# Kernel tuning notes

Hardware: AMD Instinct MI355X
Metric: run time of the kernel (lower is better)

## Reference

```python
import jax, jax.numpy as jnp
import numpy as np

DIM = 128
NUM_HEADS = 4
WS = (2, 7, 7)  # window size (D, H, W)
N = WS[0] * WS[1] * WS[2]  # 98 tokens per window
NW = 64    # number of windows per sample (mask.shape[0])
BATCH = 64
B_ = BATCH * NW


def _relative_position_index(ws):
    # replicates the numpy index construction in build()
    coords = np.stack(np.meshgrid(np.arange(ws[0]), np.arange(ws[1]), np.arange(ws[2]), indexing='ij'))
    flat = coords.reshape(3, -1)  # (3, N)
    rel = flat[:, :, None] - flat[:, None, :]  # (3, N, N)
    rel = rel.transpose(1, 2, 0).astype(np.int64)
    rel[:, :, 0] += ws[0] - 1
    rel[:, :, 1] += ws[1] - 1
    rel[:, :, 2] += ws[2] - 1
    rel[:, :, 0] *= (2 * ws[1] - 1) * (2 * ws[2] - 1)
    rel[:, :, 1] *= 2 * ws[2] - 1
    return rel.sum(-1)  # (N, N)


def setup_inputs() -> dict:
    key = jax.random.key(0)
    ks = jax.random.split(key, 8)
    C = DIM
    num_bias = (2 * WS[0] - 1) * (2 * WS[1] - 1) * (2 * WS[2] - 1)  # 507
    x = jax.random.normal(ks[0], (B_, N, C), dtype=jnp.float32)
    mask = jax.random.normal(ks[1], (NW, N, N), dtype=jnp.float32)
    qkv_w = jax.random.normal(ks[2], (C, 3 * C), dtype=jnp.float32) * (C ** -0.5)
    qkv_b = jnp.zeros((3 * C,), dtype=jnp.float32)
    proj_w = jax.random.normal(ks[3], (C, C), dtype=jnp.float32) * (C ** -0.5)
    proj_b = jnp.zeros((C,), dtype=jnp.float32)
    bias_table = jax.random.normal(ks[4], (num_bias, NUM_HEADS), dtype=jnp.float32) * 0.02
    rel_index = jnp.asarray(_relative_position_index(WS), dtype=jnp.int32)  # (N, N)
    return {"x": x, "mask": mask, "qkv_w": qkv_w, "qkv_b": qkv_b,
            "proj_w": proj_w, "proj_b": proj_b, "bias_table": bias_table,
            "rel_index": rel_index}


def reference(x, mask, qkv_w, qkv_b, proj_w, proj_b, bias_table, rel_index):
    B_all, n, C = x.shape
    H = NUM_HEADS
    hd = C // H
    scale = hd ** -0.5
    # qkv projection -> (3, B, H, N, hd)
    qkv = (x @ qkv_w + qkv_b).reshape(B_all, n, 3, H, hd).transpose(2, 0, 3, 1, 4)
    q, k, v = qkv[0], qkv[1], qkv[2]
    attn = jnp.einsum('bhnd,bhmd->bhnm', q * scale, k)  # (B, H, N, N)
    # gathered relative position bias: (N*N, H) -> (H, N, N)
    bias = bias_table[rel_index.reshape(-1)].reshape(n, n, H).transpose(2, 0, 1)
    attn = attn + bias[None]
    nW = mask.shape[0]
    attn = attn.reshape(-1, nW, H, n, n) + mask[None, :, None, :, :]
    attn = jax.nn.softmax(attn.reshape(-1, H, n, n), axis=-1)
    out = jnp.einsum('bhnm,bhmd->bhnd', attn, v)
    out = out.transpose(0, 2, 1, 3).reshape(B_all, n, C)
    return out @ proj_w + proj_b
```

## Files before the change

### kernel.cpp

```cpp
#include <hip/hip_runtime.h>

typedef __bf16 bf16x8 __attribute__((ext_vector_type(8)));
typedef __bf16 bf16x4 __attribute__((ext_vector_type(4)));
typedef __bf16 bf16x2 __attribute__((ext_vector_type(2)));
typedef float f32x4 __attribute__((ext_vector_type(4)));
typedef short short4v __attribute__((ext_vector_type(4)));
typedef int i32x2 __attribute__((ext_vector_type(2)));
typedef unsigned u32x2 __attribute__((ext_vector_type(2)));
typedef unsigned u32x4 __attribute__((ext_vector_type(4)));

#define NTOK 98
#define CDIM 128
#define SM_TOTAL 57344
#define QSCALE 0.2550181952219662f
#define LOG2E  1.4426950408889634f

#if defined(__has_builtin)
#if __has_builtin(__builtin_amdgcn_exp2f)
#define EXP2F(x) __builtin_amdgcn_exp2f(x)
#else
#define EXP2F(x) exp2f(x)
#endif
#if __has_builtin(__builtin_amdgcn_rcpf)
#define RCPF(x) __builtin_amdgcn_rcpf(x)
#else
#define RCPF(x) (1.f / (x))
#endif
#else
#define EXP2F(x) exp2f(x)
#define RCPF(x) (1.f / (x))
#endif

__device__ __forceinline__ f32x4 mfma32(bf16x8 a, bf16x8 b, f32x4 c) {
  return __builtin_amdgcn_mfma_f32_16x16x32_bf16(a, b, c, 0, 0, 0);
}

__device__ __forceinline__ f32x4 mfma16(bf16x4 a, bf16x4 b, f32x4 c) {
#if defined(__has_builtin) && __has_builtin(__builtin_amdgcn_mfma_f32_16x16x16bf16_1k)
  return __builtin_amdgcn_mfma_f32_16x16x16bf16_1k(__builtin_bit_cast(short4v, a),
                                                   __builtin_bit_cast(short4v, b), c, 0, 0, 0);
#elif defined(__has_builtin) && __has_builtin(__builtin_amdgcn_mfma_f32_16x16x16_bf16)
  return __builtin_amdgcn_mfma_f32_16x16x16_bf16(a, b, c, 0, 0, 0);
#else
  f32x4 d;
  i32x2 ai = __builtin_bit_cast(i32x2, a), bi = __builtin_bit_cast(i32x2, b);
  asm volatile("v_mfma_f32_16x16x16_bf16 %0, %1, %2, %3"
               : "=&v"(d) : "v"(ai), "v"(bi), "v"(c));
  return d;
#endif
}

__device__ __forceinline__ unsigned pk2(float a, float b) {
  bf16x2 t; t[0] = (__bf16)a; t[1] = (__bf16)b;
  return __builtin_bit_cast(unsigned, t);
}

__global__ void precompute_k(const float* __restrict__ qkv_w, const float* __restrict__ proj_w,
                             const float* __restrict__ bias_table, const int* __restrict__ rel_index,
                             const float* __restrict__ mask,
                             __bf16* __restrict__ wkT, __bf16* __restrict__ wvf,
                             __bf16* __restrict__ wqT, __bf16* __restrict__ wproj,
                             float* __restrict__ biasf, float* __restrict__ maskf) {
  int t = blockIdx.x * blockDim.x + threadIdx.x;
  int stride = gridDim.x * blockDim.x;
  for (int g = t; g < 8 * 4 * 64; g += stride) {
    int cb = g >> 8, kk = (g >> 6) & 3, lane = g & 63;
    int co = cb * 16 + (lane & 15);
    int ci0 = kk * 32 + (lane >> 4) * 8;
    __bf16 *dq = wqT + g * 8, *dk = wkT + g * 8, *dv = wvf + g * 8;
#pragma unroll
    for (int e = 0; e < 8; ++e) {
      const float* r = qkv_w + (size_t)(ci0 + e) * 384;
      dq[e] = (__bf16)r[co];
      dk[e] = (__bf16)r[128 + co];
      dv[e] = (__bf16)r[256 + co];
    }
  }
  for (int g = t; g < 8 * 4 * 64; g += stride) {
    int nt = g >> 8, kk = (g >> 6) & 3, lane = g & 63;
    int n = nt * 16 + (lane & 15);
    int k0 = kk * 32 + (lane >> 4) * 8;
    __bf16* dst = wproj + g * 8;
#pragma unroll
    for (int e = 0; e < 8; ++e) dst[e] = (__bf16)proj_w[(k0 + e) * 128 + n];
  }
  for (int g = t; g < 4 * 49 * 64; g += stride) {
    int h = g / (49 * 64), r = g % (49 * 64);
    int m = r / (7 * 64), r2 = r % (7 * 64);
    int nt = r2 / 64, lane = r2 % 64;
    int q = m * 16 + (lane & 15), k0 = nt * 16 + (lane >> 4) * 4;
    float* dst = biasf + g * 4;
#pragma unroll
    for (int j = 0; j < 4; ++j) {
      int key = k0 + j;
      dst[j] = (key < NTOK && q < NTOK) ? bias_table[rel_index[q * NTOK + key] * 4 + h] * LOG2E : 0.f;
    }
  }
  for (int g = t; g < 64 * 49 * 64; g += stride) {
    int wm = g / (49 * 64), r = g % (49 * 64);
    int m = r / (7 * 64), r2 = r % (7 * 64);
    int nt = r2 / 64, lane = r2 % 64;
    int q = m * 16 + (lane & 15), k0 = nt * 16 + (lane >> 4) * 4;
    float* dst = maskf + g * 4;
#pragma unroll
    for (int j = 0; j < 4; ++j) {
      int key = k0 + j;
      float v;
      if (key >= NTOK) v = -1e30f;
      else if (q >= NTOK) v = 0.f;
      else v = mask[wm * (NTOK * NTOK) + q * NTOK + key] * LOG2E;
      dst[j] = v;
    }
  }
}

__launch_bounds__(512, 4)
__global__ void wattn_k(const float* __restrict__ x,
                        const float* __restrict__ qkv_b, const float* __restrict__ proj_b,
                        const __bf16* __restrict__ wkT, const __bf16* __restrict__ wvf,
                        const __bf16* __restrict__ wqT, const __bf16* __restrict__ wproj,
                        const float* __restrict__ biasf, const float* __restrict__ maskf,
                        float* __restrict__ out) {
  extern __shared__ char smem[];
  __bf16* const Kf  = (__bf16*)smem;
  __bf16* const Vtf = (__bf16*)(smem + 28672);

  const int b    = blockIdx.x;
  const int tid  = threadIdx.x;
  const int w    = tid >> 6;
  const int lane = tid & 63;
  const int l15  = lane & 15;
  const int l4   = lane >> 4;
  const float* xw = x + (size_t)b * (NTOK * CDIM);

  const bool act = (w < 7);
  const int m    = act ? w : 0;
  const int mb   = m << 4;

  bf16x8 bq[4];
  if (act) {
    bf16x8 xf[4];
    {
      int row = mb + l15;
      int rowc = (row < NTOK) ? row : (NTOK - 1);
      const float* xrow = xw + (size_t)rowc * CDIM;
#pragma unroll
      for (int kk = 0; kk < 4; ++kk) {
        float4 u0 = *(const float4*)(xrow + kk * 32 + l4 * 8);
        float4 u1 = *(const float4*)(xrow + kk * 32 + l4 * 8 + 4);
        bf16x8 v;
        v[0] = (__bf16)u0.x; v[1] = (__bf16)u0.y; v[2] = (__bf16)u0.z; v[3] = (__bf16)u0.w;
        v[4] = (__bf16)u1.x; v[5] = (__bf16)u1.y; v[6] = (__bf16)u1.z; v[7] = (__bf16)u1.w;
        xf[kk] = v;
      }
    }
    {
      unsigned pk[8][2];
#pragma unroll
      for (int cbl = 0; cbl < 8; ++cbl) {
        float4 qb4 = *(const float4*)(qkv_b + cbl * 16 + (l4 << 2));
        f32x4 acc = {qb4.x, qb4.y, qb4.z, qb4.w};
#pragma unroll
        for (int kk = 0; kk < 4; ++kk) {
          bf16x8 wq8 = *(const bf16x8*)(wqT + ((cbl * 4 + kk) * 64 + lane) * 8);
          acc = mfma32(wq8, xf[kk], acc);
        }
        pk[cbl][0] = pk2(acc[0] * QSCALE, acc[1] * QSCALE);
        pk[cbl][1] = pk2(acc[2] * QSCALE, acc[3] * QSCALE);
      }
#pragma unroll
      for (int h = 0; h < 4; ++h) {
        unsigned d[4];
#pragma unroll
        for (int dd = 0; dd < 4; ++dd) {
          int srcl = (((l4 & 1) * 2 + (dd >> 1)) * 16 + l15) << 2;
          unsigned lo = (unsigned)__builtin_amdgcn_ds_bpermute(srcl, (int)pk[h * 2][dd & 1]);
          unsigned hi = (unsigned)__builtin_amdgcn_ds_bpermute(srcl, (int)pk[h * 2 + 1][dd & 1]);
          d[dd] = (l4 >= 2) ? hi : lo;
        }
        u32x4 du = {d[0], d[1], d[2], d[3]};
        bq[h] = __builtin_bit_cast(bf16x8, du);
      }
    }
#pragma unroll 1
    for (int cb = 0; cb < 8; ++cb) {
      float4 bk4 = *(const float4*)(qkv_b + 128 + cb * 16 + (l4 << 2));
      f32x4 ak = {bk4.x, bk4.y, bk4.z, bk4.w};
      float bv1 = qkv_b[256 + cb * 16 + l15];
      f32x4 av = {bv1, bv1, bv1, bv1};
#pragma unroll
      for (int kk = 0; kk < 4; ++kk) {
        bf16x8 wk8 = *(const bf16x8*)(wkT + ((cb * 4 + kk) * 64 + lane) * 8);
        bf16x8 wv8 = *(const bf16x8*)(wvf + ((cb * 4 + kk) * 64 + lane) * 8);
        ak = mfma32(wk8, xf[kk], ak);
        av = mfma32(xf[kk], wv8, av);
      }
      {
        u32x2 u; u[0] = pk2(ak[0], ak[1]); u[1] = pk2(ak[2], ak[3]);
        int idx = ((m * 4 + (cb >> 1)) * 64 + ((cb & 1) * 2 + (l4 >> 1)) * 16 + l15) * 8 + (l4 & 1) * 4;
        *reinterpret_cast<u32x2*>(Kf + idx) = u;
      }
      {
        u32x2 u; u[0] = pk2(av[0], av[1]); u[1] = pk2(av[2], av[3]);
        int idx = ((m * 8 + cb) * 64 + lane) * 4;
        *reinterpret_cast<u32x2*>(Vtf + idx) = u;
      }
    }
  }
  __syncthreads();

  u32x2 accOp[4][2];
  if (act) {
    const int wm = b & 63;
    const float* mrow = maskf + ((size_t)(wm * 49 + m * 7)) * 256 + lane * 4;
#pragma unroll
    for (int h = 0; h < 4; ++h) {
      const float* brow = biasf + ((size_t)(h * 49 + m * 7)) * 256 + lane * 4;
      bf16x4 pw[7];
      float rsum = 0.f;
#pragma unroll
      for (int nt = 0; nt < 7; ++nt) {
        f32x4 c4 = *(const f32x4*)(mrow + nt * 256);
        bf16x8 ak8 = *(const bf16x8*)(Kf + ((nt * 4 + h) * 64 + lane) * 8);
        f32x4 s = mfma32(ak8, bq[h], c4);
        f32x4 bb = *(const f32x4*)(brow + nt * 256);
        float p0 = EXP2F(s[0] + bb[0]), p1 = EXP2F(s[1] + bb[1]);
        float p2 = EXP2F(s[2] + bb[2]), p3 = EXP2F(s[3] + bb[3]);
        rsum += (p0 + p1) + (p2 + p3);
        u32x2 u; u[0] = pk2(p0, p1); u[1] = pk2(p2, p3);
        pw[nt] = __builtin_bit_cast(bf16x4, u);
      }
      rsum += __shfl_xor(rsum, 16, 64);
      rsum += __shfl_xor(rsum, 32, 64);
      float inv = RCPF(rsum);
#pragma unroll
      for (int cb2 = 0; cb2 < 2; ++cb2) {
        f32x4 acc = {0.f, 0.f, 0.f, 0.f};
#pragma unroll
        for (int nt = 0; nt < 7; ++nt) {
          bf16x4 vb = *(const bf16x4*)(Vtf + ((nt * 8 + h * 2 + cb2) * 64 + lane) * 4);
          acc = mfma16(vb, pw[nt], acc);
        }
        u32x2 u; u[0] = pk2(acc[0] * inv, acc[1] * inv); u[1] = pk2(acc[2] * inv, acc[3] * inv);
        accOp[h][cb2] = u;
      }
    }
  }
  __syncthreads();
  if (act) {
    int row = mb + l15;
    unsigned swz = (unsigned)((row & 7) << 4);
#pragma unroll
    for (int h = 0; h < 4; ++h) {
#pragma unroll
      for (int cb2 = 0; cb2 < 2; ++cb2) {
        unsigned boff = (unsigned)(row * 256 + (h * 32 + cb2 * 16 + l4 * 4) * 2) ^ swz;
        *reinterpret_cast<u32x2*>(smem + boff) = accOp[h][cb2];
      }
    }
  }
  __syncthreads();

  {
    float* outw = out + (size_t)b * (NTOK * CDIM);
    int mt = w % 7, nt2 = w / 7;
    for (int pt = w; pt < 28; pt += 8) {
      const int mb3 = mt << 4;
      const int ntA = nt2 << 1;
      int row = mb3 + l15;
      unsigned swz = (unsigned)((row & 7) << 4);
      f32x4 accA = {0.f, 0.f, 0.f, 0.f};
      f32x4 accB = {0.f, 0.f, 0.f, 0.f};
#pragma unroll
      for (int kk = 0; kk < 4; ++kk) {
        unsigned boff = (unsigned)(row * 256 + kk * 64 + l4 * 16) ^ swz;
        bf16x8 a  = *(const bf16x8*)(smem + boff);
        bf16x8 b0 = *(const bf16x8*)(wproj + (((ntA << 2) + kk) * 64 + lane) * 8);
        bf16x8 b1 = *(const bf16x8*)(wproj + ((((ntA + 1) << 2) + kk) * 64 + lane) * 8);
        accA = mfma32(a, b0, accA);
        accB = mfma32(a, b1, accB);
      }
#pragma unroll
      for (int u = 0; u < 2; ++u) {
        f32x4 acc = u ? accB : accA;
        int n = ((ntA + u) << 4) + l15;
        float pb = proj_b[n];
#pragma unroll
        for (int j = 0; j < 4; ++j) {
          int i = mb3 + (l4 << 2) + j;
          if (i < NTOK) outw[i * CDIM + n] = acc[j] + pb;
        }
      }
      mt += 1; nt2 += 1;
      if (mt >= 7) { mt -= 7; ++nt2; }
    }
  }
}

extern "C" void kernel_launch(void* const* d_in, const int* in_sizes, int n_in,
                              void* d_out, int out_size, void* d_ws, size_t ws_size,
                              hipStream_t stream) {
  const float* x        = (const float*)d_in[0];
  const float* mask     = (const float*)d_in[1];
  const float* qkv_w    = (const float*)d_in[2];
  const float* qkv_b    = (const float*)d_in[3];
  const float* proj_w   = (const float*)d_in[4];
  const float* proj_b   = (const float*)d_in[5];
  const float* bias_tab = (const float*)d_in[6];
  const int*   rel_idx  = (const int*)d_in[7];
  float* out = (float*)d_out;

  char* ws = (char*)d_ws;
  __bf16* wkT   = (__bf16*)(ws + 0);
  __bf16* wvf   = (__bf16*)(ws + 32768);
  __bf16* wqT   = (__bf16*)(ws + 65536);
  __bf16* wproj = (__bf16*)(ws + 98304);
  float*  biasf = (float*)(ws + 131072);
  float*  maskf = (float*)(ws + 331776);

  precompute_k<<<512, 256, 0, stream>>>(qkv_w, proj_w, bias_tab, rel_idx, mask,
                                        wkT, wvf, wqT, wproj, biasf, maskf);

  hipFuncSetAttribute(reinterpret_cast<const void*>(wattn_k),
                      hipFuncAttributeMaxDynamicSharedMemorySize, SM_TOTAL);
  wattn_k<<<4096, 512, SM_TOTAL, stream>>>(x, qkv_b, proj_b, wkT, wvf, wqT, wproj,
                                           biasf, maskf, out);
}
```

Before: 242.3 us.

## Fold bias into per-head mask table and prefetch head-0 tile early

```diff
diff --git a/kernel.cpp b/kernel.cpp
--- a/kernel.cpp
+++ b/kernel.cpp
@@ -60,7 +60,7 @@
                              const float* __restrict__ mask,
                              __bf16* __restrict__ wkT, __bf16* __restrict__ wvf,
                              __bf16* __restrict__ wqT, __bf16* __restrict__ wproj,
-                             float* __restrict__ biasf, float* __restrict__ maskf) {
+                             float* __restrict__ combf) {
   int t = blockIdx.x * blockDim.x + threadIdx.x;
   int stride = gridDim.x * blockDim.x;
   for (int g = t; g < 8 * 4 * 64; g += stride) {
@@ -84,31 +84,22 @@
 #pragma unroll
     for (int e = 0; e < 8; ++e) dst[e] = (__bf16)proj_w[(k0 + e) * 128 + n];
   }
-  for (int g = t; g < 4 * 49 * 64; g += stride) {
-    int h = g / (49 * 64), r = g % (49 * 64);
-    int m = r / (7 * 64), r2 = r % (7 * 64);
-    int nt = r2 / 64, lane = r2 % 64;
+  for (int g = t; g < 4 * 64 * 49 * 64; g += stride) {
+    int lane = g & 63;
+    int r = g >> 6;
+    int mnt = r % 49;
+    int hw = r / 49;
+    int wm = hw & 63, h = hw >> 6;
+    int m = mnt / 7, nt = mnt % 7;
     int q = m * 16 + (lane & 15), k0 = nt * 16 + (lane >> 4) * 4;
-    float* dst = biasf + g * 4;
-#pragma unroll
-    for (int j = 0; j < 4; ++j) {
-      int key = k0 + j;
-      dst[j] = (key < NTOK && q < NTOK) ? bias_table[rel_index[q * NTOK + key] * 4 + h] * LOG2E : 0.f;
-    }
-  }
-  for (int g = t; g < 64 * 49 * 64; g += stride) {
-    int wm = g / (49 * 64), r = g % (49 * 64);
-    int m = r / (7 * 64), r2 = r % (7 * 64);
-    int nt = r2 / 64, lane = r2 % 64;
-    int q = m * 16 + (lane & 15), k0 = nt * 16 + (lane >> 4) * 4;
-    float* dst = maskf + g * 4;
+    float* dst = combf + (size_t)g * 4;
 #pragma unroll
     for (int j = 0; j < 4; ++j) {
       int key = k0 + j;
       float v;
       if (key >= NTOK) v = -1e30f;
       else if (q >= NTOK) v = 0.f;
-      else v = mask[wm * (NTOK * NTOK) + q * NTOK + key] * LOG2E;
+      else v = (bias_table[rel_index[q * NTOK + key] * 4 + h] + mask[wm * (NTOK * NTOK) + q * NTOK + key]) * LOG2E;
       dst[j] = v;
     }
   }
@@ -119,7 +110,7 @@
                         const float* __restrict__ qkv_b, const float* __restrict__ proj_b,
                         const __bf16* __restrict__ wkT, const __bf16* __restrict__ wvf,
                         const __bf16* __restrict__ wqT, const __bf16* __restrict__ wproj,
-                        const float* __restrict__ biasf, const float* __restrict__ maskf,
+                        const float* __restrict__ combf,
                         float* __restrict__ out) {
   extern __shared__ char smem[];
   __bf16* const Kf  = (__bf16*)smem;
@@ -132,13 +123,20 @@
   const int l15  = lane & 15;
   const int l4   = lane >> 4;
   const float* xw = x + (size_t)b * (NTOK * CDIM);
+  const int wm   = b & 63;
 
   const bool act = (w < 7);
   const int m    = act ? w : 0;
   const int mb   = m << 4;
 
   bf16x8 bq[4];
+  f32x4 c4h0[7];
   if (act) {
+    {
+      const float* crow0 = combf + (((size_t)(0 * 64 + wm) * 49) + m * 7) * 256 + lane * 4;
+#pragma unroll
+      for (int nt = 0; nt < 7; ++nt) c4h0[nt] = *(const f32x4*)(crow0 + nt * 256);
+    }
     bf16x8 xf[4];
     {
       int row = mb + l15;
@@ -182,7 +180,7 @@
         bq[h] = __builtin_bit_cast(bf16x8, du);
       }
     }
-#pragma unroll 1
+#pragma unroll 2
     for (int cb = 0; cb < 8; ++cb) {
       float4 bk4 = *(const float4*)(qkv_b + 128 + cb * 16 + (l4 << 2));
       f32x4 ak = {bk4.x, bk4.y, bk4.z, bk4.w};
@@ -211,21 +209,25 @@
 
   u32x2 accOp[4][2];
   if (act) {
-    const int wm = b & 63;
-    const float* mrow = maskf + ((size_t)(wm * 49 + m * 7)) * 256 + lane * 4;
 #pragma unroll
     for (int h = 0; h < 4; ++h) {
-      const float* brow = biasf + ((size_t)(h * 49 + m * 7)) * 256 + lane * 4;
+      f32x4 cc[7];
+      if (h == 0) {
+#pragma unroll
+        for (int nt = 0; nt < 7; ++nt) cc[nt] = c4h0[nt];
+      } else {
+        const float* crow = combf + (((size_t)(h * 64 + wm) * 49) + m * 7) * 256 + lane * 4;
+#pragma unroll
+        for (int nt = 0; nt < 7; ++nt) cc[nt] = *(const f32x4*)(crow + nt * 256);
+      }
       bf16x4 pw[7];
       float rsum = 0.f;
 #pragma unroll
       for (int nt = 0; nt < 7; ++nt) {
-        f32x4 c4 = *(const f32x4*)(mrow + nt * 256);
         bf16x8 ak8 = *(const bf16x8*)(Kf + ((nt * 4 + h) * 64 + lane) * 8);
-        f32x4 s = mfma32(ak8, bq[h], c4);
-        f32x4 bb = *(const f32x4*)(brow + nt * 256);
-        float p0 = EXP2F(s[0] + bb[0]), p1 = EXP2F(s[1] + bb[1]);
-        float p2 = EXP2F(s[2] + bb[2]), p3 = EXP2F(s[3] + bb[3]);
+        f32x4 s = mfma32(ak8, bq[h], cc[nt]);
+        float p0 = EXP2F(s[0]), p1 = EXP2F(s[1]);
+        float p2 = EXP2F(s[2]), p3 = EXP2F(s[3]);
         rsum += (p0 + p1) + (p2 + p3);
         u32x2 u; u[0] = pk2(p0, p1); u[1] = pk2(p2, p3);
         pw[nt] = __builtin_bit_cast(bf16x4, u);
@@ -235,12 +237,19 @@
       float inv = RCPF(rsum);
 #pragma unroll
       for (int cb2 = 0; cb2 < 2; ++cb2) {
-        f32x4 acc = {0.f, 0.f, 0.f, 0.f};
-#pragma unroll
-        for (int nt = 0; nt < 7; ++nt) {
+        f32x4 accA = {0.f, 0.f, 0.f, 0.f};
+        f32x4 accB = {0.f, 0.f, 0.f, 0.f};
+#pragma unroll
+        for (int nt = 0; nt < 4; ++nt) {
           bf16x4 vb = *(const bf16x4*)(Vtf + ((nt * 8 + h * 2 + cb2) * 64 + lane) * 4);
-          acc = mfma16(vb, pw[nt], acc);
-        }
+          accA = mfma16(vb, pw[nt], accA);
+        }
+#pragma unroll
+        for (int nt = 4; nt < 7; ++nt) {
+          bf16x4 vb = *(const bf16x4*)(Vtf + ((nt * 8 + h * 2 + cb2) * 64 + lane) * 4);
+          accB = mfma16(vb, pw[nt], accB);
+        }
+        f32x4 acc = accA + accB;
         u32x2 u; u[0] = pk2(acc[0] * inv, acc[1] * inv); u[1] = pk2(acc[2] * inv, acc[3] * inv);
         accOp[h][cb2] = u;
       }
@@ -315,14 +324,13 @@
   __bf16* wvf   = (__bf16*)(ws + 32768);
   __bf16* wqT   = (__bf16*)(ws + 65536);
   __bf16* wproj = (__bf16*)(ws + 98304);
-  float*  biasf = (float*)(ws + 131072);
-  float*  maskf = (float*)(ws + 331776);
+  float*  combf = (float*)(ws + 131072);
 
   precompute_k<<<512, 256, 0, stream>>>(qkv_w, proj_w, bias_tab, rel_idx, mask,
-                                        wkT, wvf, wqT, wproj, biasf, maskf);
+                                        wkT, wvf, wqT, wproj, combf);
 
   hipFuncSetAttribute(reinterpret_cast<const void*>(wattn_k),
                       hipFuncAttributeMaxDynamicSharedMemorySize, SM_TOTAL);
   wattn_k<<<4096, 512, SM_TOTAL, stream>>>(x, qkv_b, proj_b, wkT, wvf, wqT, wproj,
-                                           biasf, maskf, out);
-}
+                                           combf, out);
+}
```

New measurement: 266.5 us. 1.1x slower.

## Keep attention output in registers for projection, drop idle wave and barriers

Applied to the files above, without the earlier changes.

```diff
diff --git a/kernel.cpp b/kernel.cpp
--- a/kernel.cpp
+++ b/kernel.cpp
@@ -55,6 +55,20 @@
   return __builtin_bit_cast(unsigned, t);
 }
 
+#define TRANSPOSE_CD_TO_AFRAG(dst, src0, src1)                                          \
+  {                                                                                     \
+    unsigned d_[4];                                                                     \
+    _Pragma("unroll")                                                                   \
+    for (int dd = 0; dd < 4; ++dd) {                                                    \
+      int srcl_ = (((l4 & 1) * 2 + (dd >> 1)) * 16 + l15) << 2;                         \
+      unsigned lo_ = (unsigned)__builtin_amdgcn_ds_bpermute(srcl_, (int)(src0)[dd & 1]);\
+      unsigned hi_ = (unsigned)__builtin_amdgcn_ds_bpermute(srcl_, (int)(src1)[dd & 1]);\
+      d_[dd] = (l4 >= 2) ? hi_ : lo_;                                                   \
+    }                                                                                   \
+    u32x4 du_ = {d_[0], d_[1], d_[2], d_[3]};                                           \
+    dst = __builtin_bit_cast(bf16x8, du_);                                              \
+  }
+
 __global__ void precompute_k(const float* __restrict__ qkv_w, const float* __restrict__ proj_w,
                              const float* __restrict__ bias_table, const int* __restrict__ rel_index,
                              const float* __restrict__ mask,
@@ -114,7 +128,7 @@
   }
 }
 
-__launch_bounds__(512, 4)
+__launch_bounds__(448, 4)
 __global__ void wattn_k(const float* __restrict__ x,
                         const float* __restrict__ qkv_b, const float* __restrict__ proj_b,
                         const __bf16* __restrict__ wkT, const __bf16* __restrict__ wvf,
@@ -132,13 +146,13 @@
   const int l15  = lane & 15;
   const int l4   = lane >> 4;
   const float* xw = x + (size_t)b * (NTOK * CDIM);
-
-  const bool act = (w < 7);
-  const int m    = act ? w : 0;
-  const int mb   = m << 4;
+  const int wm   = b & 63;
+
+  const int m  = w;
+  const int mb = m << 4;
 
   bf16x8 bq[4];
-  if (act) {
+  {
     bf16x8 xf[4];
     {
       int row = mb + l15;
@@ -169,18 +183,8 @@
         pk[cbl][1] = pk2(acc[2] * QSCALE, acc[3] * QSCALE);
       }
 #pragma unroll
-      for (int h = 0; h < 4; ++h) {
-        unsigned d[4];
-#pragma unroll
-        for (int dd = 0; dd < 4; ++dd) {
-          int srcl = (((l4 & 1) * 2 + (dd >> 1)) * 16 + l15) << 2;
-          unsigned lo = (unsigned)__builtin_amdgcn_ds_bpermute(srcl, (int)pk[h * 2][dd & 1]);
-          unsigned hi = (unsigned)__builtin_amdgcn_ds_bpermute(srcl, (int)pk[h * 2 + 1][dd & 1]);
-          d[dd] = (l4 >= 2) ? hi : lo;
-        }
-        u32x4 du = {d[0], d[1], d[2], d[3]};
-        bq[h] = __builtin_bit_cast(bf16x8, du);
-      }
+      for (int h = 0; h < 4; ++h)
+        TRANSPOSE_CD_TO_AFRAG(bq[h], pk[h * 2], pk[h * 2 + 1]);
     }
 #pragma unroll 1
     for (int cb = 0; cb < 8; ++cb) {
@@ -210,8 +214,7 @@
   __syncthreads();
 
   u32x2 accOp[4][2];
-  if (act) {
-    const int wm = b & 63;
+  {
     const float* mrow = maskf + ((size_t)(wm * 49 + m * 7)) * 256 + lane * 4;
 #pragma unroll
     for (int h = 0; h < 4; ++h) {
@@ -235,50 +238,44 @@
       float inv = RCPF(rsum);
 #pragma unroll
       for (int cb2 = 0; cb2 < 2; ++cb2) {
-        f32x4 acc = {0.f, 0.f, 0.f, 0.f};
-#pragma unroll
-        for (int nt = 0; nt < 7; ++nt) {
+        f32x4 accA = {0.f, 0.f, 0.f, 0.f};
+        f32x4 accB = {0.f, 0.f, 0.f, 0.f};
+#pragma unroll
+        for (int nt = 0; nt < 4; ++nt) {
           bf16x4 vb = *(const bf16x4*)(Vtf + ((nt * 8 + h * 2 + cb2) * 64 + lane) * 4);
-          acc = mfma16(vb, pw[nt], acc);
+          accA = mfma16(vb, pw[nt], accA);
         }
+#pragma unroll
+        for (int nt = 4; nt < 7; ++nt) {
+          bf16x4 vb = *(const bf16x4*)(Vtf + ((nt * 8 + h * 2 + cb2) * 64 + lane) * 4);
+          accB = mfma16(vb, pw[nt], accB);
+        }
+        f32x4 acc = accA + accB;
         u32x2 u; u[0] = pk2(acc[0] * inv, acc[1] * inv); u[1] = pk2(acc[2] * inv, acc[3] * inv);
         accOp[h][cb2] = u;
       }
     }
   }
-  __syncthreads();
-  if (act) {
-    int row = mb + l15;
-    unsigned swz = (unsigned)((row & 7) << 4);
-#pragma unroll
-    for (int h = 0; h < 4; ++h) {
-#pragma unroll
-      for (int cb2 = 0; cb2 < 2; ++cb2) {
-        unsigned boff = (unsigned)(row * 256 + (h * 32 + cb2 * 16 + l4 * 4) * 2) ^ swz;
-        *reinterpret_cast<u32x2*>(smem + boff) = accOp[h][cb2];
-      }
-    }
-  }
-  __syncthreads();
 
   {
+    bf16x8 af[4];
+#pragma unroll
+    for (int kk = 0; kk < 4; ++kk)
+      TRANSPOSE_CD_TO_AFRAG(af[kk], accOp[kk][0], accOp[kk][1]);
+
     float* outw = out + (size_t)b * (NTOK * CDIM);
-    int mt = w % 7, nt2 = w / 7;
-    for (int pt = w; pt < 28; pt += 8) {
-      const int mb3 = mt << 4;
-      const int ntA = nt2 << 1;
-      int row = mb3 + l15;
-      unsigned swz = (unsigned)((row & 7) << 4);
+    const int rlim = NTOK - mb;
+#pragma unroll
+    for (int p = 0; p < 4; ++p) {
+      const int ntA = p << 1;
       f32x4 accA = {0.f, 0.f, 0.f, 0.f};
       f32x4 accB = {0.f, 0.f, 0.f, 0.f};
 #pragma unroll
       for (int kk = 0; kk < 4; ++kk) {
-        unsigned boff = (unsigned)(row * 256 + kk * 64 + l4 * 16) ^ swz;
-        bf16x8 a  = *(const bf16x8*)(smem + boff);
         bf16x8 b0 = *(const bf16x8*)(wproj + (((ntA << 2) + kk) * 64 + lane) * 8);
         bf16x8 b1 = *(const bf16x8*)(wproj + ((((ntA + 1) << 2) + kk) * 64 + lane) * 8);
-        accA = mfma32(a, b0, accA);
-        accB = mfma32(a, b1, accB);
+        accA = mfma32(af[kk], b0, accA);
+        accB = mfma32(af[kk], b1, accB);
       }
 #pragma unroll
       for (int u = 0; u < 2; ++u) {
@@ -287,12 +284,10 @@
         float pb = proj_b[n];
 #pragma unroll
         for (int j = 0; j < 4; ++j) {
-          int i = mb3 + (l4 << 2) + j;
-          if (i < NTOK) outw[i * CDIM + n] = acc[j] + pb;
+          int i = (l4 << 2) + j;
+          if (i < rlim) outw[(mb + i) * CDIM + n] = acc[j] + pb;
         }
       }
-      mt += 1; nt2 += 1;
-      if (mt >= 7) { mt -= 7; ++nt2; }
     }
   }
 }
@@ -323,6 +318,6 @@
 
   hipFuncSetAttribute(reinterpret_cast<const void*>(wattn_k),
                       hipFuncAttributeMaxDynamicSharedMemorySize, SM_TOTAL);
-  wattn_k<<<4096, 512, SM_TOTAL, stream>>>(x, qkv_b, proj_b, wkT, wvf, wqT, wproj,
+  wattn_k<<<4096, 448, SM_TOTAL, stream>>>(x, qkv_b, proj_b, wkT, wvf, wqT, wproj,
                                            biasf, maskf, out);
 }
```

After: 281.2 us. +16.0%, slower.
